# Performance work log

Measured on AMD Instinct MI355X. Metric: run time of the kernel, lower is better.

## Reference

```python
import jax, jax.numpy as jnp
import numpy as np
from jax import lax

NPOINT = 1024
K = 32
EPS = 1e-5  # BatchNorm eps (eval mode, running stats)


def _fps(xyz, npoint):
    """Farthest point sampling. xyz: [B,N,3] -> idx [B,npoint] (int32).
    Deterministic start at index 0 (torch version starts at a random index)."""
    B, N, _ = xyz.shape
    barange = jnp.arange(B)

    def step(carry, _):
        distance, farthest = carry
        centroid = xyz[barange, farthest]                    # [B,3]
        d = jnp.sum((xyz - centroid[:, None, :]) ** 2, -1)   # [B,N]
        distance = jnp.minimum(distance, d)
        new_far = jnp.argmax(distance, axis=-1).astype(jnp.int32)
        return (distance, new_far), farthest

    init = (jnp.full((B, N), 1e10, dtype=xyz.dtype), jnp.zeros((B,), jnp.int32))
    _, centroids = lax.scan(step, init, None, length=npoint)  # [npoint,B]
    return centroids.T                                        # [B,npoint]


def _square_distance(src, dst):
    # src [B,M,3], dst [B,N,3] -> [B,M,N]
    return (jnp.sum(src ** 2, -1)[:, :, None]
            - 2.0 * jnp.einsum('bmc,bnc->bmn', src, dst)
            + jnp.sum(dst ** 2, -1)[:, None, :])


def _gather(p, idx):
    # p [B,N,C], idx [B,...] -> [B,...,C]
    return jax.vmap(lambda pb, ib: pb[ib])(p, idx)


def _mlp_layer(x, w, cb, g, b, m, v):
    # x [B,S,K,Cin]; Conv2d 1x1 == channel matmul, then eval-mode BN, ReLU
    x = jnp.einsum('bskc,oc->bsko', x, w) + cb
    x = (x - m) * (g / jnp.sqrt(v + EPS)) + b
    return jax.nn.relu(x)


def _forward(xyz, points, w0, cb0, g0, b0, m0, v0,
             w1, cb1, g1, b1, m1, v1, w2, cb2, g2, b2, m2, v2):
    fps_idx = _fps(xyz, NPOINT)                       # [B,S]
    new_xyz = _gather(xyz, fps_idx)                   # [B,S,3]
    dists = _square_distance(new_xyz, xyz)            # [B,S,N]
    _, nn_idx = lax.top_k(-dists, K)                  # [B,S,K]
    grouped_xyz = _gather(xyz, nn_idx)                # [B,S,K,3]
    grouped_xyz_norm = grouped_xyz - new_xyz[:, :, None, :]
    grouped_pts = _gather(points, nn_idx)             # [B,S,K,C]
    x = jnp.concatenate([grouped_xyz_norm, grouped_pts], axis=-1)  # [B,S,K,3+C]
    x = _mlp_layer(x, w0, cb0, g0, b0, m0, v0)
    x = _mlp_layer(x, w1, cb1, g1, b1, m1, v1)
    x = _mlp_layer(x, w2, cb2, g2, b2, m2, v2)
    new_points = jnp.max(x, axis=2)                   # max over K -> [B,S,Cout]
    return new_xyz, jnp.transpose(new_points, (0, 2, 1))  # [B,Cout,S]


def setup_inputs() -> dict:
    key = jax.random.key(0)
    ks = jax.random.split(key, 8)
    B, N, C = 16, 4096, 64
    inp = {
        'xyz': jax.random.normal(ks[0], (B, N, 3), jnp.float32),
        'points': jax.random.normal(ks[1], (B, N, C), jnp.float32),
    }
    channels = [(3 + C, 64), (64, 64), (64, 128)]
    for li, (ci, co) in enumerate(channels):
        inp[f'w{li}'] = jax.random.normal(ks[2 + li], (co, ci), jnp.float32) * 0.05
        inp[f'cb{li}'] = jnp.zeros((co,), jnp.float32)
        inp[f'g{li}'] = jnp.ones((co,), jnp.float32)
        inp[f'b{li}'] = jnp.zeros((co,), jnp.float32)
        inp[f'm{li}'] = jnp.zeros((co,), jnp.float32)
        inp[f'v{li}'] = jnp.ones((co,), jnp.float32)
    return inp


def reference(xyz, points, w0, cb0, g0, b0, m0, v0,
              w1, cb1, g1, b1, m1, v1, w2, cb2, g2, b2, m2, v2):
    return _forward(xyz, points, w0, cb0, g0, b0, m0, v0,
                    w1, cb1, g1, b1, m1, v1, w2, cb2, g2, b2, m2, v2)
```

## Files before the change

### kernel.cpp

```cpp
#include <hip/hip_runtime.h>
#include <math.h>

#define NPTS 4096
#define NB 16
#define NS 1024
#define KNB 32
#define CPTS 64

#define FLAG_OFF_B  0
#define CNT_OFF_B   64
#define PUBC_OFF_B  128
#define WFRAG_ELEMS 18432
#define NGROUPS     2048

typedef __attribute__((ext_vector_type(8))) short short8;
typedef __attribute__((ext_vector_type(4))) float f32x4;

__device__ __forceinline__ short f2bf(float f) {
  unsigned u = __float_as_uint(f);
  unsigned r = (u + 0x7fffu + ((u >> 16) & 1u)) >> 16;
  return (short)r;
}

template <int CTRL>
__device__ __forceinline__ int dppmov(int cur) {
  return __builtin_amdgcn_update_dpp(cur, cur, CTRL, 0xF, 0xF, false);
}
template <int CTRL>
__device__ __forceinline__ void dpp_min_u64(unsigned& hi, unsigned& lo) {
  unsigned nhi = (unsigned)dppmov<CTRL>((int)hi);
  unsigned nlo = (unsigned)dppmov<CTRL>((int)lo);
  bool lt = (nhi < hi) || (nhi == hi && nlo < lo);
  hi = lt ? nhi : hi;
  lo = lt ? nlo : lo;
}
template <int CTRL>
__device__ __forceinline__ void dpp_fmax(float& m) {
  m = fmaxf(m, __int_as_float(dppmov<CTRL>(__float_as_int(m))));
}
template <int CTRL>
__device__ __forceinline__ void dpp_umin(unsigned& v) {
  unsigned o = (unsigned)dppmov<CTRL>((int)v);
  v = (o < v) ? o : v;
}

#define XSTR 104
__global__ __launch_bounds__(512, 2) void fused_kernel(
    const float* __restrict__ xyz, const float* __restrict__ points,
    const float* __restrict__ w0, const float* __restrict__ cb0, const float* __restrict__ g0,
    const float* __restrict__ b0, const float* __restrict__ m0, const float* __restrict__ v0,
    const float* __restrict__ w1, const float* __restrict__ cb1, const float* __restrict__ g1,
    const float* __restrict__ b1, const float* __restrict__ m1, const float* __restrict__ v1,
    const float* __restrict__ w2, const float* __restrict__ cb2, const float* __restrict__ g2,
    const float* __restrict__ b2, const float* __restrict__ m2, const float* __restrict__ v2,
    char* __restrict__ wsb, float* __restrict__ newxyz, float* __restrict__ outp) {
  struct FpsSh {
    float4 sxyz4[NPTS];
    float4 centL[NS];
    unsigned long long part[2][8];
  };
  struct WorkerSh {
    short Wlds[WFRAG_ELEMS];
    union {
      unsigned long long slist[2][4096];
      short X[8][32 * XSTR];
    } u;
    unsigned long long wl[2][128];
    int nnL[8][KNB];
    float biasL[256];
    float pubq[8][3];
    unsigned gshare;
  };
  __shared__ union { FpsSh f; WorkerSh w; } sh;

  const int t = threadIdx.x;
  const int lane = t & 63;
  const int wave = t >> 6;
  unsigned* flagp = (unsigned*)(wsb + FLAG_OFF_B);
  unsigned* cntp  = (unsigned*)(wsb + CNT_OFF_B);
  float* pubC = (float*)(wsb + PUBC_OFF_B);

  if (blockIdx.x < NB) {
    const int b = blockIdx.x;
    const float* xb = xyz + (size_t)b * NPTS * 3;
    float* outb = newxyz + (size_t)b * NS * 3;

    for (int i = t; i < NPTS; i += 512)
      sh.f.sxyz4[i] = make_float4(xb[i * 3 + 0], xb[i * 3 + 1], xb[i * 3 + 2], 0.f);

    float px[8], py[8], pz[8], dist[8];
#pragma unroll
    for (int j = 0; j < 8; ++j) {
      int n = t + 512 * j;
      px[j] = xb[n * 3 + 0];
      py[j] = xb[n * 3 + 1];
      pz[j] = xb[n * 3 + 2];
      dist[j] = 1e10f;
    }
    __syncthreads();
    float cx = sh.f.sxyz4[0].x, cy = sh.f.sxyz4[0].y, cz = sh.f.sxyz4[0].z;
    if (t == 0) sh.f.centL[0] = sh.f.sxyz4[0];

    for (int it = 1; it < NS; ++it) {
      const int buf = it & 1;
      float dm[8];
#pragma unroll
      for (int j = 0; j < 8; ++j) {
        float dx = __fsub_rn(px[j], cx);
        float dy = __fsub_rn(py[j], cy);
        float dz = __fsub_rn(pz[j], cz);
        float d  = __fadd_rn(__fadd_rn(__fmul_rn(dx, dx), __fmul_rn(dy, dy)), __fmul_rn(dz, dz));
        float v  = fminf(dist[j], d);
        dist[j] = v;
        dm[j] = v;
      }
      float m = fmaxf(fmaxf(fmaxf(dm[0], dm[1]), fmaxf(dm[2], dm[3])),
                      fmaxf(fmaxf(dm[4], dm[5]), fmaxf(dm[6], dm[7])));
      dpp_fmax<0xB1>(m);  dpp_fmax<0x4E>(m);  dpp_fmax<0x141>(m);
      dpp_fmax<0x140>(m); dpp_fmax<0x142>(m); dpp_fmax<0x143>(m);
      float M = __int_as_float(__builtin_amdgcn_readlane(__float_as_int(m), 63));
      unsigned idxl = 0xFFFFFFFFu;
#pragma unroll
      for (int j = 7; j >= 0; --j) idxl = (dm[j] == M) ? (unsigned)(t + 512 * j) : idxl;
      dpp_umin<0xB1>(idxl);  dpp_umin<0x4E>(idxl);  dpp_umin<0x141>(idxl);
      dpp_umin<0x140>(idxl); dpp_umin<0x142>(idxl); dpp_umin<0x143>(idxl);
      if (lane == 63)
        sh.f.part[buf][wave] = ((unsigned long long)__float_as_uint(M) << 32) | (unsigned)(~idxl);
      __syncthreads();
      unsigned long long k0 = sh.f.part[buf][0];
#pragma unroll
      for (int w = 1; w < 8; ++w) {
        unsigned long long kw = sh.f.part[buf][w];
        k0 = (kw > k0) ? kw : k0;
      }
      int bi = (int)(~(unsigned)k0) & 4095;
      float4 c4 = sh.f.sxyz4[bi];
      cx = c4.x; cy = c4.y; cz = c4.z;
      if (t == 0) sh.f.centL[it] = c4;
      if ((it & 31) == 31 && wave == 0) {
        if (lane == 0)
          __hip_atomic_store(&flagp[b], (unsigned)(it - 31), __ATOMIC_RELEASE, __HIP_MEMORY_SCOPE_AGENT);
        if (lane < 32) {
          int ci = it - 31 + lane;
          float4 cc = sh.f.centL[ci];
          float* dst = pubC + ((size_t)b * NS + ci) * 3;
          __hip_atomic_store(dst + 0, cc.x, __ATOMIC_RELAXED, __HIP_MEMORY_SCOPE_AGENT);
          __hip_atomic_store(dst + 1, cc.y, __ATOMIC_RELAXED, __HIP_MEMORY_SCOPE_AGENT);
          __hip_atomic_store(dst + 2, cc.z, __ATOMIC_RELAXED, __HIP_MEMORY_SCOPE_AGENT);
        }
      }
    }
    if (wave == 0 && lane == 0)
      __hip_atomic_store(&flagp[b], (unsigned)NS, __ATOMIC_RELEASE, __HIP_MEMORY_SCOPE_AGENT);
    __syncthreads();
    const float* cf = (const float*)sh.f.centL;
    for (int i = t; i < NS * 3; i += 512) {
      int p = i / 3, c = i - p * 3;
      outb[i] = cf[p * 4 + c];
    }
  }

  __syncthreads();
  for (int i = t; i < WFRAG_ELEMS; i += 512) {
    int g = i >> 9, ln = (i >> 3) & 63, j = i & 7;
    int l, nt, s;
    if (g < 12)      { l = 0; nt = g / 3;  s = g % 3; }
    else if (g < 20) { l = 1; int gg = g - 12; nt = gg >> 1; s = gg & 1; }
    else             { l = 2; int gg = g - 20; nt = gg >> 1; s = gg & 1; }
    int n = nt * 16 + (ln & 15);
    int k = s * 32 + ((ln >> 4) << 3) + j;
    float val = 0.f;
    if (l == 0) { if (k < 67) val = w0[n * 67 + k] * (g0[n] / sqrtf(v0[n] + 1e-5f)); }
    else if (l == 1) { val = w1[n * 64 + k] * (g1[n] / sqrtf(v1[n] + 1e-5f)); }
    else { val = w2[n * 64 + k] * (g2[n] / sqrtf(v2[n] + 1e-5f)); }
    sh.w.Wlds[i] = f2bf(val);
  }
  if (t < 256) {
    int o = t;
    float bv;
    if (o < 64)       { float sc = g0[o] / sqrtf(v0[o] + 1e-5f); bv = (cb0[o] - m0[o]) * sc + b0[o]; }
    else if (o < 128) { int c = o - 64;  float sc = g1[c] / sqrtf(v1[c] + 1e-5f); bv = (cb1[c] - m1[c]) * sc + b1[c]; }
    else              { int c = o - 128; float sc = g2[c] / sqrtf(v2[c] + 1e-5f); bv = (cb2[c] - m2[c]) * sc + b2[c]; }
    sh.w.biasL[o] = bv;
  }
  const int team = t >> 8, tt = t & 255;

  for (;;) {
    __syncthreads();
    if (t == 0) sh.w.gshare = atomicAdd(cntp, 1u);
    __syncthreads();
    unsigned g = sh.w.gshare;
    if (g >= NGROUPS) break;
    const int b = (int)(g & 15u);
    const int s0 = (int)(g >> 4) << 3;

    if (t == 0) {
      unsigned need = (unsigned)(s0 + 8);
      for (;;) {
        unsigned f = __hip_atomic_load(&flagp[b], __ATOMIC_ACQUIRE, __HIP_MEMORY_SCOPE_AGENT);
        if (f >= need) break;
        __builtin_amdgcn_s_sleep(8);
      }
    }
    __syncthreads();
    if (t < 24)
      sh.w.pubq[t / 3][t % 3] = __hip_atomic_load(
          &pubC[((size_t)b * NS + s0 + t / 3) * 3 + (t % 3)],
          __ATOMIC_RELAXED, __HIP_MEMORY_SCOPE_AGENT);
    __syncthreads();

    const float* xb = xyz + (size_t)b * NPTS * 3;

    for (int sub = 0; sub < 4; ++sub) {
      const int qi = team * 4 + sub;
      float qx = sh.w.pubq[qi][0], qy = sh.w.pubq[qi][1], qz = sh.w.pubq[qi][2];
      float s2 = __fadd_rn(__fadd_rn(__fmul_rn(qx, qx), __fmul_rn(qy, qy)), __fmul_rn(qz, qz));
      unsigned long long key[16];
#pragma unroll
      for (int j = 0; j < 16; ++j) {
        int n = tt + 256 * j;
        float px = xb[n * 3], py = xb[n * 3 + 1], pz = xb[n * 3 + 2];
        float n2 = __fadd_rn(__fadd_rn(__fmul_rn(px, px), __fmul_rn(py, py)), __fmul_rn(pz, pz));
        float dt = __fadd_rn(__fadd_rn(__fmul_rn(qx, px), __fmul_rn(qy, py)), __fmul_rn(qz, pz));
        float d  = __fadd_rn(__fsub_rn(s2, __fmul_rn(2.0f, dt)), n2);
        unsigned u = __float_as_uint(d);
        u ^= (0x80000000u | (unsigned)((int)u >> 31));
        key[j] = ((unsigned long long)u << 32) | (unsigned)n;
      }
#pragma unroll
      for (int p = 1; p < 16; p <<= 1) {
#pragma unroll
        for (int k = p; k >= 1; k >>= 1) {
#pragma unroll
          for (int j = k % p; j + k < 16; j += 2 * k) {
#pragma unroll
            for (int i = 0; i < k; ++i) {
              if (i + j + k < 16 && (i + j) / (2 * p) == (i + j + k) / (2 * p)) {
                unsigned long long ka = key[i + j], kb = key[i + j + k];
                unsigned long long mn = ka < kb ? ka : kb;
                unsigned long long mx = ka < kb ? kb : ka;
                key[i + j] = mn; key[i + j + k] = mx;
              }
            }
          }
        }
      }
#pragma unroll
      for (int i = 0; i < 16; ++i) sh.w.u.slist[team][i * 256 + tt] = key[i];

      unsigned long long head = key[0];
      unsigned long long nxt  = key[1];
      unsigned p = 1;
      for (int r = 0; r < KNB; ++r) {
        unsigned hi = (unsigned)(head >> 32), lo = (unsigned)head;
        dpp_min_u64<0xB1>(hi, lo);
        dpp_min_u64<0x4E>(hi, lo);
        dpp_min_u64<0x141>(hi, lo);
        dpp_min_u64<0x140>(hi, lo);
        dpp_min_u64<0x142>(hi, lo);
        dpp_min_u64<0x143>(hi, lo);
        unsigned whi = (unsigned)__builtin_amdgcn_readlane((int)hi, 63);
        unsigned wlo = (unsigned)__builtin_amdgcn_readlane((int)lo, 63);
        unsigned long long wkey = ((unsigned long long)whi << 32) | wlo;
        if ((tt & 63) == 0) sh.w.wl[team][(tt >> 6) * 32 + r] = wkey;
        if (head == wkey) {
          head = (p < 16) ? nxt : 0xFFFFFFFFFFFFFFFFull;
          unsigned pn = p + 1;
          nxt = sh.w.u.slist[team][(pn < 16 ? pn : 15) * 256 + tt];
          p = pn;
        }
      }
      __syncthreads();
      if (tt < 128) {
        unsigned long long mykey = sh.w.wl[team][tt];
        int gr = 0;
#pragma unroll 8
        for (int i = 0; i < 128; ++i) gr += (sh.w.wl[team][i] < mykey) ? 1 : 0;
        if (gr < KNB) sh.w.nnL[qi][gr] = (int)(mykey & 0xFFFFFFFFull);
      }
      __syncthreads();
    }

    {
      const int qi = wave;
      const int s = s0 + qi;
      float qx = sh.w.pubq[qi][0], qy = sh.w.pubq[qi][1], qz = sh.w.pubq[qi][2];
      const float* pb = points + (size_t)b * NPTS * CPTS;
      const float* bias = sh.w.biasL;
      short* X = sh.w.u.X[qi];

      {
        int r = lane & 31, half = lane >> 5;
        int idx = sh.w.nnL[qi][r];
        const float* prow = pb + (size_t)idx * CPTS;
#pragma unroll
        for (int i = 0; i < 48; ++i) {
          int c = half * 48 + i;
          float v;
          if (c < 3) {
            float qc = (c == 0) ? qx : ((c == 1) ? qy : qz);
            v = __fsub_rn(xb[idx * 3 + c], qc);
          } else if (c < 67) {
            v = prow[c - 3];
          } else {
            v = 0.f;
          }
          X[r * XSTR + c] = f2bf(v);
        }
      }

      const int ml = lane & 15, quad = lane >> 4;
      const short8* Wf = (const short8*)sh.w.Wlds;

      short8 a0[2][3];
#pragma unroll
      for (int m2 = 0; m2 < 2; ++m2)
#pragma unroll
        for (int s3 = 0; s3 < 3; ++s3)
          a0[m2][s3] = *(const short8*)&X[(m2 * 16 + ml) * XSTR + s3 * 32 + quad * 8];
      f32x4 acc0[2][4];
#pragma unroll
      for (int m2 = 0; m2 < 2; ++m2)
#pragma unroll
        for (int nt = 0; nt < 4; ++nt) {
          f32x4 c = {0.f, 0.f, 0.f, 0.f};
#pragma unroll
          for (int s3 = 0; s3 < 3; ++s3)
            c = __builtin_amdgcn_mfma_f32_16x16x32_bf16(a0[m2][s3], Wf[(nt * 3 + s3) * 64 + lane], c, 0, 0, 0);
          acc0[m2][nt] = c;
        }
#pragma unroll
      for (int m2 = 0; m2 < 2; ++m2)
#pragma unroll
        for (int nt = 0; nt < 4; ++nt) {
          int ch = nt * 16 + ml;
          float bv = bias[ch];
#pragma unroll
          for (int r4 = 0; r4 < 4; ++r4) {
            float y = fmaxf(acc0[m2][nt][r4] + bv, 0.f);
            int m = quad * 4 + r4;
            int sK = ch >> 5, qq = (ch >> 3) & 3, jj = ch & 7;
            X[((m2 * 2 + sK) * 64 + qq * 16 + m) * 8 + jj] = f2bf(y);
          }
        }

      short8 a1[2][2];
#pragma unroll
      for (int m2 = 0; m2 < 2; ++m2)
#pragma unroll
        for (int sK = 0; sK < 2; ++sK)
          a1[m2][sK] = *(const short8*)&X[((m2 * 2 + sK) * 64 + lane) * 8];
      f32x4 acc1[2][4];
#pragma unroll
      for (int m2 = 0; m2 < 2; ++m2)
#pragma unroll
        for (int nt = 0; nt < 4; ++nt) {
          f32x4 c = {0.f, 0.f, 0.f, 0.f};
#pragma unroll
          for (int sK = 0; sK < 2; ++sK)
            c = __builtin_amdgcn_mfma_f32_16x16x32_bf16(a1[m2][sK], Wf[(12 + nt * 2 + sK) * 64 + lane], c, 0, 0, 0);
          acc1[m2][nt] = c;
        }
#pragma unroll
      for (int m2 = 0; m2 < 2; ++m2)
#pragma unroll
        for (int nt = 0; nt < 4; ++nt) {
          int ch = nt * 16 + ml;
          float bv = bias[64 + ch];
#pragma unroll
          for (int r4 = 0; r4 < 4; ++r4) {
            float y = fmaxf(acc1[m2][nt][r4] + bv, 0.f);
            int m = quad * 4 + r4;
            int sK = ch >> 5, qq = (ch >> 3) & 3, jj = ch & 7;
            X[((m2 * 2 + sK) * 64 + qq * 16 + m) * 8 + jj] = f2bf(y);
          }
        }

      short8 a2[2][2];
#pragma unroll
      for (int m2 = 0; m2 < 2; ++m2)
#pragma unroll
        for (int sK = 0; sK < 2; ++sK)
          a2[m2][sK] = *(const short8*)&X[((m2 * 2 + sK) * 64 + lane) * 8];
#pragma unroll
      for (int nt = 0; nt < 8; ++nt) {
        f32x4 c0 = {0.f, 0.f, 0.f, 0.f}, c1 = {0.f, 0.f, 0.f, 0.f};
        short8 w0f = Wf[(20 + nt * 2 + 0) * 64 + lane];
        short8 w1f = Wf[(20 + nt * 2 + 1) * 64 + lane];
        c0 = __builtin_amdgcn_mfma_f32_16x16x32_bf16(a2[0][0], w0f, c0, 0, 0, 0);
        c0 = __builtin_amdgcn_mfma_f32_16x16x32_bf16(a2[0][1], w1f, c0, 0, 0, 0);
        c1 = __builtin_amdgcn_mfma_f32_16x16x32_bf16(a2[1][0], w0f, c1, 0, 0, 0);
        c1 = __builtin_amdgcn_mfma_f32_16x16x32_bf16(a2[1][1], w1f, c1, 0, 0, 0);
        float bv = bias[128 + nt * 16 + ml];
        float m = -1.f;
#pragma unroll
        for (int r4 = 0; r4 < 4; ++r4) {
          m = fmaxf(m, fmaxf(c0[r4] + bv, 0.f));
          m = fmaxf(m, fmaxf(c1[r4] + bv, 0.f));
        }
        m = fmaxf(m, __shfl_xor(m, 16, 64));
        m = fmaxf(m, __shfl_xor(m, 32, 64));
        if (lane < 16) outp[((size_t)b * 128 + nt * 16 + lane) * NS + s] = m;
      }
    }
  }
}

extern "C" void kernel_launch(void* const* d_in, const int* in_sizes, int n_in,
                              void* d_out, int out_size, void* d_ws, size_t ws_size,
                              hipStream_t stream) {
  const float* xyz    = (const float*)d_in[0];
  const float* points = (const float*)d_in[1];
  const float* w0  = (const float*)d_in[2];
  const float* cb0 = (const float*)d_in[3];
  const float* g0  = (const float*)d_in[4];
  const float* b0  = (const float*)d_in[5];
  const float* m0  = (const float*)d_in[6];
  const float* v0  = (const float*)d_in[7];
  const float* w1  = (const float*)d_in[8];
  const float* cb1 = (const float*)d_in[9];
  const float* g1  = (const float*)d_in[10];
  const float* b1  = (const float*)d_in[11];
  const float* m1  = (const float*)d_in[12];
  const float* v1  = (const float*)d_in[13];
  const float* w2  = (const float*)d_in[14];
  const float* cb2 = (const float*)d_in[15];
  const float* g2  = (const float*)d_in[16];
  const float* b2  = (const float*)d_in[17];
  const float* m2  = (const float*)d_in[18];
  const float* v2  = (const float*)d_in[19];

  char*  wsb    = (char*)d_ws;
  float* newxyz = (float*)d_out;
  float* outp   = (float*)d_out + (size_t)NB * NS * 3;

  hipMemsetAsync(wsb, 0, 128, stream);
  fused_kernel<<<256, 512, 0, stream>>>(
      xyz, points, w0, cb0, g0, b0, m0, v0, w1, cb1, g1, b1, m1, v1,
      w2, cb2, g2, b2, m2, v2, wsb, newxyz, outp);
}
```

Measured before the change: 911.8 us.

## Run FPS on four waves with fused max-index DPP reduction

The farthest-point-sampling loop now runs on only four waves, each thread holding 16 points instead of 8. Waves 4-7 just take part in the matching barriers. The separate max-then-argmin reductions are merged into one packed 64-bit (distance, ~index) DPP max reduction, which removes the readlane and the second DPP chain. The cross-wave combine now reads 4 partials through DPP instead of a serial loop over 8. This aims to shorten the per-iteration critical path on the serial FPS loop, at the cost of more per-thread ALU work and higher register use.

```diff
diff --git a/kernel.cpp b/kernel.cpp
--- a/kernel.cpp
+++ b/kernel.cpp
@@ -35,13 +35,12 @@
   lo = lt ? nlo : lo;
 }
 template <int CTRL>
-__device__ __forceinline__ void dpp_fmax(float& m) {
-  m = fmaxf(m, __int_as_float(dppmov<CTRL>(__float_as_int(m))));
-}
-template <int CTRL>
-__device__ __forceinline__ void dpp_umin(unsigned& v) {
-  unsigned o = (unsigned)dppmov<CTRL>((int)v);
-  v = (o < v) ? o : v;
+__device__ __forceinline__ void dpp_max_u64(unsigned& hi, unsigned& lo) {
+  unsigned nhi = (unsigned)dppmov<CTRL>((int)hi);
+  unsigned nlo = (unsigned)dppmov<CTRL>((int)lo);
+  bool gt = (nhi > hi) || (nhi == hi && nlo > lo);
+  hi = gt ? nhi : hi;
+  lo = gt ? nlo : lo;
 }
 
 #define XSTR 104
@@ -57,7 +56,7 @@
   struct FpsSh {
     float4 sxyz4[NPTS];
     float4 centL[NS];
-    unsigned long long part[2][8];
+    unsigned long long part[2][4];
   };
   struct WorkerSh {
     short Wlds[WFRAG_ELEMS];
@@ -88,71 +87,89 @@
     for (int i = t; i < NPTS; i += 512)
       sh.f.sxyz4[i] = make_float4(xb[i * 3 + 0], xb[i * 3 + 1], xb[i * 3 + 2], 0.f);
 
-    float px[8], py[8], pz[8], dist[8];
-#pragma unroll
-    for (int j = 0; j < 8; ++j) {
-      int n = t + 512 * j;
-      px[j] = xb[n * 3 + 0];
-      py[j] = xb[n * 3 + 1];
-      pz[j] = xb[n * 3 + 2];
-      dist[j] = 1e10f;
+    if (wave < 4) {
+      float px[16], py[16], pz[16], dist[16];
+#pragma unroll
+      for (int j = 0; j < 16; ++j) {
+        int n = t + 256 * j;
+        px[j] = xb[n * 3 + 0];
+        py[j] = xb[n * 3 + 1];
+        pz[j] = xb[n * 3 + 2];
+        dist[j] = 1e10f;
+      }
+      __syncthreads();
+      float cx = sh.f.sxyz4[0].x, cy = sh.f.sxyz4[0].y, cz = sh.f.sxyz4[0].z;
+      if (t == 0) sh.f.centL[0] = sh.f.sxyz4[0];
+
+      for (int it = 1; it < NS; ++it) {
+        const int buf = it & 1;
+        float dm[16];
+#pragma unroll
+        for (int j = 0; j < 16; ++j) {
+          float dx = __fsub_rn(px[j], cx);
+          float dy = __fsub_rn(py[j], cy);
+          float dz = __fsub_rn(pz[j], cz);
+          float d  = __fadd_rn(__fadd_rn(__fmul_rn(dx, dx), __fmul_rn(dy, dy)), __fmul_rn(dz, dz));
+          float v  = fminf(dist[j], d);
+          dist[j] = v;
+          dm[j] = v;
+        }
+        float t8[8], t4a[4];
+#pragma unroll
+        for (int k = 0; k < 8; ++k) t8[k] = fmaxf(dm[k], dm[k + 8]);
+#pragma unroll
+        for (int k = 0; k < 4; ++k) t4a[k] = fmaxf(t8[k], t8[k + 4]);
+        float M = fmaxf(fmaxf(t4a[0], t4a[1]), fmaxf(t4a[2], t4a[3]));
+        unsigned c8[8], c4a[4];
+#pragma unroll
+        for (int k = 0; k < 8; ++k) {
+          unsigned a = (dm[k] == M)     ? (unsigned)(t + 256 * k)       : 0xFFFFFFFFu;
+          unsigned bq = (dm[k + 8] == M) ? (unsigned)(t + 256 * (k + 8)) : 0xFFFFFFFFu;
+          c8[k] = a < bq ? a : bq;
+        }
+#pragma unroll
+        for (int k = 0; k < 4; ++k) c4a[k] = c8[k] < c8[k + 4] ? c8[k] : c8[k + 4];
+        unsigned i2a = c4a[0] < c4a[2] ? c4a[0] : c4a[2];
+        unsigned i2b = c4a[1] < c4a[3] ? c4a[1] : c4a[3];
+        unsigned il = i2a < i2b ? i2a : i2b;
+        unsigned hi = __float_as_uint(M), lo = ~il;
+        dpp_max_u64<0xB1>(hi, lo);
+        dpp_max_u64<0x4E>(hi, lo);
+        dpp_max_u64<0x141>(hi, lo);
+        dpp_max_u64<0x140>(hi, lo);
+        dpp_max_u64<0x142>(hi, lo);
+        dpp_max_u64<0x143>(hi, lo);
+        if (lane == 63) sh.f.part[buf][wave] = ((unsigned long long)hi << 32) | lo;
+        __syncthreads();
+        unsigned long long k0 = sh.f.part[buf][lane & 3];
+        unsigned khi = (unsigned)(k0 >> 32), klo = (unsigned)k0;
+        dpp_max_u64<0xB1>(khi, klo);
+        dpp_max_u64<0x4E>(khi, klo);
+        int bi = (int)(~klo) & 4095;
+        float4 c4v = sh.f.sxyz4[bi];
+        cx = c4v.x; cy = c4v.y; cz = c4v.z;
+        if (t == 0) sh.f.centL[it] = c4v;
+        if ((it & 31) == 31 && wave == 0) {
+          if (lane == 0)
+            __hip_atomic_store(&flagp[b], (unsigned)(it - 31), __ATOMIC_RELEASE, __HIP_MEMORY_SCOPE_AGENT);
+          if (lane < 32) {
+            int ci = it - 31 + lane;
+            float4 cc = sh.f.centL[ci];
+            float* dst = pubC + ((size_t)b * NS + ci) * 3;
+            __hip_atomic_store(dst + 0, cc.x, __ATOMIC_RELAXED, __HIP_MEMORY_SCOPE_AGENT);
+            __hip_atomic_store(dst + 1, cc.y, __ATOMIC_RELAXED, __HIP_MEMORY_SCOPE_AGENT);
+            __hip_atomic_store(dst + 2, cc.z, __ATOMIC_RELAXED, __HIP_MEMORY_SCOPE_AGENT);
+          }
+        }
+      }
+      if (t == 0)
+        __hip_atomic_store(&flagp[b], (unsigned)NS, __ATOMIC_RELEASE, __HIP_MEMORY_SCOPE_AGENT);
+      __syncthreads();
+    } else {
+      __syncthreads();
+      for (int it = 1; it < NS; ++it) __syncthreads();
+      __syncthreads();
     }
-    __syncthreads();
-    float cx = sh.f.sxyz4[0].x, cy = sh.f.sxyz4[0].y, cz = sh.f.sxyz4[0].z;
-    if (t == 0) sh.f.centL[0] = sh.f.sxyz4[0];
-
-    for (int it = 1; it < NS; ++it) {
-      const int buf = it & 1;
-      float dm[8];
-#pragma unroll
-      for (int j = 0; j < 8; ++j) {
-        float dx = __fsub_rn(px[j], cx);
-        float dy = __fsub_rn(py[j], cy);
-        float dz = __fsub_rn(pz[j], cz);
-        float d  = __fadd_rn(__fadd_rn(__fmul_rn(dx, dx), __fmul_rn(dy, dy)), __fmul_rn(dz, dz));
-        float v  = fminf(dist[j], d);
-        dist[j] = v;
-        dm[j] = v;
-      }
-      float m = fmaxf(fmaxf(fmaxf(dm[0], dm[1]), fmaxf(dm[2], dm[3])),
-                      fmaxf(fmaxf(dm[4], dm[5]), fmaxf(dm[6], dm[7])));
-      dpp_fmax<0xB1>(m);  dpp_fmax<0x4E>(m);  dpp_fmax<0x141>(m);
-      dpp_fmax<0x140>(m); dpp_fmax<0x142>(m); dpp_fmax<0x143>(m);
-      float M = __int_as_float(__builtin_amdgcn_readlane(__float_as_int(m), 63));
-      unsigned idxl = 0xFFFFFFFFu;
-#pragma unroll
-      for (int j = 7; j >= 0; --j) idxl = (dm[j] == M) ? (unsigned)(t + 512 * j) : idxl;
-      dpp_umin<0xB1>(idxl);  dpp_umin<0x4E>(idxl);  dpp_umin<0x141>(idxl);
-      dpp_umin<0x140>(idxl); dpp_umin<0x142>(idxl); dpp_umin<0x143>(idxl);
-      if (lane == 63)
-        sh.f.part[buf][wave] = ((unsigned long long)__float_as_uint(M) << 32) | (unsigned)(~idxl);
-      __syncthreads();
-      unsigned long long k0 = sh.f.part[buf][0];
-#pragma unroll
-      for (int w = 1; w < 8; ++w) {
-        unsigned long long kw = sh.f.part[buf][w];
-        k0 = (kw > k0) ? kw : k0;
-      }
-      int bi = (int)(~(unsigned)k0) & 4095;
-      float4 c4 = sh.f.sxyz4[bi];
-      cx = c4.x; cy = c4.y; cz = c4.z;
-      if (t == 0) sh.f.centL[it] = c4;
-      if ((it & 31) == 31 && wave == 0) {
-        if (lane == 0)
-          __hip_atomic_store(&flagp[b], (unsigned)(it - 31), __ATOMIC_RELEASE, __HIP_MEMORY_SCOPE_AGENT);
-        if (lane < 32) {
-          int ci = it - 31 + lane;
-          float4 cc = sh.f.centL[ci];
-          float* dst = pubC + ((size_t)b * NS + ci) * 3;
-          __hip_atomic_store(dst + 0, cc.x, __ATOMIC_RELAXED, __HIP_MEMORY_SCOPE_AGENT);
-          __hip_atomic_store(dst + 1, cc.y, __ATOMIC_RELAXED, __HIP_MEMORY_SCOPE_AGENT);
-          __hip_atomic_store(dst + 2, cc.z, __ATOMIC_RELAXED, __HIP_MEMORY_SCOPE_AGENT);
-        }
-      }
-    }
-    if (wave == 0 && lane == 0)
-      __hip_atomic_store(&flagp[b], (unsigned)NS, __ATOMIC_RELEASE, __HIP_MEMORY_SCOPE_AGENT);
-    __syncthreads();
     const float* cf = (const float*)sh.f.centL;
     for (int i = t; i < NS * 3; i += 512) {
       int p = i / 3, c = i - p * 3;
```

Measured after the change: 956.4 us. +4.9%, slower.
